# Optimization experiments

Hardware: AMD Instinct MI355X
Metric: run time of the kernel (lower is better)

The kernel has to match this reference:

```python
import math
import jax, jax.numpy as jnp
import numpy as np

NC, NA, NL = 80, 3, 3
NO = NC + 5
STRIDES = (8, 16, 32)
BS, IN_CH, IMG, NT = 8, 256, 640, 200
BALANCE = (4.0, 1.0, 0.25)
G, ANCHOR_T, EPS = 0.5, 2.91, 1e-9
LBOX_W, LOBJ_W, LCLS_W, POS_BAL = 0.05, 1.0, 0.5, 0.5
OFF = np.array([[0., 0.], [1., 0.], [0., 1.], [-1., 0.], [0., -1.]], np.float32) * G
_h = np.sqrt(np.array([0.5, 1.0, 2.0], np.float32))  # h_ratios = sqrt(aspect_ratios)
# per layer anchors: (w, h) = (size/h_ratio, size*h_ratio), divided by stride (grid units)
ANCHORS = np.stack([np.stack([s / _h, s * _h], 1) / st
                    for s, st in zip((32., 64., 128.), STRIDES)]).astype(np.float32)  # [NL,NA,2]


def setup_inputs():
    key = jax.random.key(0)
    ks = jax.random.split(key, 16)
    inp = {}
    for i, st in enumerate(STRIDES):
        n = IMG // st
        inp[f"feat{i}"] = jax.random.normal(ks[i], (BS, IN_CH, n, n), jnp.float32)
        inp[f"w{i}"] = jax.random.normal(ks[3 + i], (NO * NA, IN_CH), jnp.float32) * 0.02
        b = np.zeros((NA, NO), np.float32)
        b[:, 4] += math.log(8 / (640 / st) ** 2)          # _initialize_biases obj prior
        b[:, 5:] += math.log(0.6 / (NC - 0.99))           # _initialize_biases cls prior
        inp[f"b{i}"] = jnp.asarray(b.reshape(-1))
    # targets: [NT, 6] = (image_idx, class, cx, cy, w, h) normalized to [0,1]
    img = jax.random.randint(ks[6], (NT, 1), 0, BS).astype(jnp.float32)
    cls = jax.random.randint(ks[7], (NT, 1), 0, NC).astype(jnp.float32)
    xy = jax.random.uniform(ks[8], (NT, 2), minval=0.05, maxval=0.95)
    wh = jax.random.uniform(ks[9], (NT, 2), minval=0.02, maxval=0.3)
    inp["targets"] = jnp.concatenate([img, cls, xy, wh], 1)
    return inp


def _head(x, w, b):
    # 1x1 conv == channel GEMM, then view/permute to [bs, na, ny, nx, no]
    y = jnp.einsum('bchw,oc->bohw', x, w) + b[None, :, None, None]
    bs, _, ny, nx = y.shape
    return y.reshape(bs, NA, NO, ny, nx).transpose(0, 1, 3, 4, 2)


def _ciou(b1, b2):
    # b1, b2: [n,4] in center-xywh format; YOLOv5-style CIoU
    x1, y1, w1, h1 = b1[:, 0], b1[:, 1], b1[:, 2], b1[:, 3]
    x2, y2, w2, h2 = b2[:, 0], b2[:, 1], b2[:, 2], b2[:, 3]
    b1x1, b1x2, b1y1, b1y2 = x1 - w1 / 2, x1 + w1 / 2, y1 - h1 / 2, y1 + h1 / 2
    b2x1, b2x2, b2y1, b2y2 = x2 - w2 / 2, x2 + w2 / 2, y2 - h2 / 2, y2 + h2 / 2
    inter = (jnp.maximum(jnp.minimum(b1x2, b2x2) - jnp.maximum(b1x1, b2x1), 0.0)
             * jnp.maximum(jnp.minimum(b1y2, b2y2) - jnp.maximum(b1y1, b2y1), 0.0))
    union = w1 * h1 + w2 * h2 - inter + EPS
    iou = inter / union
    cw = jnp.maximum(b1x2, b2x2) - jnp.minimum(b1x1, b2x1)  # enclosing box
    ch = jnp.maximum(b1y2, b2y2) - jnp.minimum(b1y1, b2y1)
    c2 = cw ** 2 + ch ** 2 + EPS
    rho2 = ((b2x1 + b2x2 - b1x1 - b1x2) ** 2 + (b2y1 + b2y2 - b1y1 - b1y2) ** 2) / 4
    v = (4.0 / math.pi ** 2) * (jnp.arctan(w2 / (h2 + EPS)) - jnp.arctan(w1 / (h1 + EPS))) ** 2
    alpha = jax.lax.stop_gradient(v / (v - iou + (1.0 + EPS)))
    return iou - (rho2 / c2 + v * alpha)


def _bce_pw(logits, t, pw):
    # BCEWithLogits with pos_weight: pw*t*(-logsigmoid(x)) + (1-t)*softplus(x)
    return pw * t * jax.nn.softplus(-logits) + (1.0 - t) * jax.nn.softplus(logits)


def _forward(feats, ws, bias, targets):
    anchors = jnp.asarray(ANCHORS)
    off = jnp.asarray(OFF)
    ai = jnp.arange(NA, dtype=jnp.float32)
    # targets replicated per anchor with anchor index appended: [NA, NT, 7]
    tg = jnp.concatenate([jnp.broadcast_to(targets[None], (NA, NT, 6)),
                          jnp.broadcast_to(ai[:, None, None], (NA, NT, 1))], 2)
    lbox = jnp.float32(0.0); lobj = jnp.float32(0.0); lcls = jnp.float32(0.0)
    for i in range(NL):
        pi = _head(feats[i], ws[i], bias[i])  # [BS, NA, ny, nx, NO]
        ny, nx = pi.shape[2], pi.shape[3]
        gain = jnp.array([1, 1, nx, ny, nx, ny, 1], jnp.float32)
        t = tg * gain  # grid units, [NA, NT, 7]
        # anchor-ratio filter (torch: t = t[j]) expressed as a validity mask
        r = t[..., 4:6] / anchors[i][:, None, :]
        m_anchor = (jnp.max(jnp.maximum(r, 1.0 / r), -1) < ANCHOR_T).reshape(-1)  # [NA*NT]
        tf = t.reshape(-1, 7)
        gxy = tf[:, 2:4]
        gxi = jnp.array([nx, ny], jnp.float32) - gxy
        near = (gxy % 1.0 < G) & (gxy > 1.0)
        far = (gxi % 1.0 < G) & (gxi > 1.0)
        sel = jnp.stack([jnp.ones_like(near[:, 0]), near[:, 0], near[:, 1], far[:, 0], far[:, 1]])
        mask = (sel & m_anchor[None]).reshape(-1)  # [5*NA*NT] valid candidates
        N = tf.shape[0]
        t5 = jnp.broadcast_to(tf[None], (5, N, 7)).reshape(-1, 7)
        offs = jnp.broadcast_to(off[:, None, :], (5, N, 2)).reshape(-1, 2)
        b_idx = t5[:, 0].astype(jnp.int32)
        c_idx = t5[:, 1].astype(jnp.int32)
        a_idx = t5[:, 6].astype(jnp.int32)
        gxy5, gwh5 = t5[:, 2:4], t5[:, 4:6]
        gij = (gxy5 - offs).astype(jnp.int32)  # trunc, values are positive -> matches .long()
        gi = jnp.clip(gij[:, 0], 0, nx - 1)
        gj = jnp.clip(gij[:, 1], 0, ny - 1)
        tbox = jnp.concatenate([gxy5 - gij.astype(jnp.float32), gwh5], 1)
        anch = anchors[i][a_idx]
        # gather predictions at sparse (b, a, gj, gi)
        ps = pi[b_idx, a_idx, gj, gi]  # [M, NO]
        pxy = jax.nn.sigmoid(ps[:, :2]) * 2.0 - 0.5
        pwh = (jax.nn.sigmoid(ps[:, 2:4]) * 2.0) ** 2 * anch
        iou = _ciou(jnp.concatenate([pxy, pwh], 1), tbox)
        fmask = mask.astype(jnp.float32)
        n_valid = fmask.sum()
        lbox = lbox + jnp.sum(fmask * (1.0 - iou)) / jnp.maximum(n_valid, 1.0)
        # scatter tobj; invalid rows routed to padded batch slot BS then sliced off
        b_s = jnp.where(mask, b_idx, BS)
        tobj = jnp.zeros((BS + 1, NA, ny, nx), jnp.float32)
        tobj = tobj.at[b_s, a_idx, gj, gi].set(
            jax.lax.stop_gradient(jnp.maximum(iou, 0.0)))[:BS]
        # classification BCE with dynamically computed pos_weight
        tcl = jax.nn.one_hot(c_idx, NC, dtype=jnp.float32)
        pw_c = (n_valid * (NC - 1)) * POS_BAL / jnp.maximum(n_valid, 2.0)
        bce_c = _bce_pw(ps[:, 5:], tcl, pw_c)
        lcls = lcls + jnp.sum(fmask[:, None] * bce_c) / jnp.maximum(n_valid * NC, 1.0)
        # objectness BCE over the full map with dynamic pos_weight
        fg_o = (tobj > 0).sum().astype(jnp.float32)
        bg_o = (tobj == 0).sum().astype(jnp.float32)
        pw_o = bg_o * POS_BAL / jnp.maximum(fg_o, 2.0)
        lobj = lobj + jnp.mean(_bce_pw(pi[..., 4], tobj, pw_o)) * BALANCE[i]
    return jnp.stack([lbox * LBOX_W, lobj * LOBJ_W, lcls * LCLS_W])


def reference(feat0, feat1, feat2, w0, w1, w2, b0, b1, b2, targets):
    return _forward((feat0, feat1, feat2), (w0, w1, w2), (b0, b1, b2), targets)
```

## Files before the change

kernel.cpp:

```cpp
#include <hip/hip_runtime.h>
#include <stdint.h>

#define NCLS 80
#define NO 85
#define CIN 256
#define ANCHOR_T 2.91f
#define EPSF 1e-9f

#define S0 153600
#define S1_ 38400
#define S2_ 9600
#define LB0 0
#define LB1 153600
#define LB2 192000

#define NGATHB 375
#define NHEADB 1050
#define NB (NGATHB + NHEADB)
#define NREC (NGATHB * 24)
#define NFIN1 96

#define WS_TOBJ_OFF 0
#define WS_HSP_OFF  806400
#define WS_GP_OFF   810608
#define WS_REC_OFF  816608
#define WS_PART_OFF 960608

__device__ __constant__ float AW_[3] = {5.656854249f, 4.0f, 2.828427125f};
__device__ __constant__ float AH_[3] = {2.828427125f, 4.0f, 5.656854249f};

__device__ __forceinline__ float softplusf(float x) {
    return fmaxf(x, 0.0f) + log1pf(expf(-fabsf(x)));
}
__device__ __forceinline__ float sigmoidf_(float x) {
    return 1.0f / (1.0f + expf(-x));
}
__device__ __forceinline__ float wave_red(float v) {
    #pragma unroll
    for (int o = 32; o > 0; o >>= 1) v += __shfl_down(v, o);
    return v;
}

struct HeadSm {
    float lw[3][CIN];
    float part[16][16][13];
    float ws_[4];
};
struct GathSm {
    float lf[8][260];
    float pb[8][3][5];
    float tbx[8][4];
    int   vm[8], eb[8], egi[8], egj[8], ec[8];
    int   kblk;
    float r1[24], r2[24];
    float wsum[2][4];
};
union AllSm { HeadSm h; GathSm g; };

template<int PERQ, int BLK0>
__device__ __forceinline__ void head_impl(
    const float* __restrict__ f, const float* __restrict__ w, const float* __restrict__ bi,
    float* __restrict__ hsp, int hb, int tid, HeadSm& sm)
{
    for (int i = tid; i < 3 * CIN; i += 256) {
        int a = i >> 8, c = i & 255;
        sm.lw[a][c] = w[(a * NO + 4) * CIN + c];
    }
    __syncthreads();

    const int q     = tid & 15;
    const int chunk = tid >> 4;
    const int qL = (hb - BLK0) * 16 + q;
    const int b  = qL / PERQ;
    const int r  = qL - b * PERQ;
    const float4* p = (const float4*)f + (b * CIN + chunk * 16) * PERQ + r;

    float acc[12];
    #pragma unroll
    for (int j = 0; j < 12; ++j) acc[j] = 0.f;

    #pragma unroll
    for (int i = 0; i < 16; ++i) {
        float4 v = p[i * PERQ];
        const int c = chunk * 16 + i;
        #pragma unroll
        for (int a = 0; a < 3; ++a) {
            float wv = sm.lw[a][c];
            acc[a*4+0] += v.x * wv;
            acc[a*4+1] += v.y * wv;
            acc[a*4+2] += v.z * wv;
            acc[a*4+3] += v.w * wv;
        }
    }

    #pragma unroll
    for (int v = 0; v < 12; ++v) sm.part[chunk][q][v] = acc[v];
    __syncthreads();

    float sp = 0.f;
    if (tid < 192) {
        int q2 = tid / 12, v = tid - q2 * 12;
        float s = 0.f;
        #pragma unroll
        for (int c2 = 0; c2 < 16; ++c2) s += sm.part[c2][q2][v];
        s += bi[(v >> 2) * NO + 4];
        sp = softplusf(s);
    }
    sp = wave_red(sp);
    if ((tid & 63) == 0) sm.ws_[tid >> 6] = sp;
    __syncthreads();
    if (tid == 0)
        hsp[hb] = sm.ws_[0] + sm.ws_[1] + sm.ws_[2] + sm.ws_[3];
}

__device__ void gath_impl(
    const float* __restrict__ f, const float* __restrict__ w, const float* __restrict__ bi,
    const float* __restrict__ targets,
    unsigned* __restrict__ tobj4, float4* __restrict__ gp, int4* __restrict__ recs,
    int bid, int tid, int l, int o, int tile, GathSm& sm)
{
    const int nx = (l == 0) ? 80 : (l == 1) ? 40 : 20;
    const int ny = nx;
    const int plane = nx * ny;
    const int ltb = (l == 0) ? LB0 : (l == 1) ? LB1 : LB2;

    if (tid < 8) {
        const int t = tid;
        const int n = tile * 8 + t;
        const float* tg = targets + n * 6;
        float tb = tg[0], tcl = tg[1];
        float gx = tg[2] * (float)nx, gy = tg[3] * (float)ny;
        float gw = tg[4] * (float)nx, gh = tg[5] * (float)ny;
        float ox = 0.f, oy = 0.f;
        bool s = true;
        if (o == 1)      { s = (fmodf(gx, 1.f) < 0.5f) && (gx > 1.f); ox = 0.5f; }
        else if (o == 2) { s = (fmodf(gy, 1.f) < 0.5f) && (gy > 1.f); oy = 0.5f; }
        else if (o == 3) { float gxi = (float)nx - gx; s = (fmodf(gxi, 1.f) < 0.5f) && (gxi > 1.f); ox = -0.5f; }
        else if (o == 4) { float gyi = (float)ny - gy; s = (fmodf(gyi, 1.f) < 0.5f) && (gyi > 1.f); oy = -0.5f; }
        int vmask = 0;
        if (s) {
            #pragma unroll
            for (int a = 0; a < 3; ++a) {
                float rw = gw / AW_[a], rh = gh / AH_[a];
                float mr = fmaxf(fmaxf(rw, 1.f / rw), fmaxf(rh, 1.f / rh));
                if (mr < ANCHOR_T) vmask |= (1 << a);
            }
        }
        sm.vm[t] = vmask;
        int gi = (int)(gx - ox);
        int gj = (int)(gy - oy);
        sm.tbx[t][0] = gx - (float)gi;
        sm.tbx[t][1] = gy - (float)gj;
        sm.tbx[t][2] = gw;
        sm.tbx[t][3] = gh;
        sm.egi[t] = min(max(gi, 0), nx - 1);
        sm.egj[t] = min(max(gj, 0), ny - 1);
        sm.eb[t]  = (int)tb;
        sm.ec[t]  = (int)tcl;
    }
    __syncthreads();

    if (tid == 0) {
        int k = 0;
        #pragma unroll
        for (int t = 0; t < 8; ++t) k |= sm.vm[t];
        sm.kblk = k;
    }
    __syncthreads();

    if (sm.kblk == 0) {
        if (tid == 0) gp[bid] = make_float4(0.f, 0.f, 0.f, 0.f);
        return;
    }

    {
        const int t  = tid >> 5;
        const int ln = tid & 31;
        if (sm.vm[t]) {
            const float* fb = f + sm.eb[t] * CIN * plane + sm.egj[t] * nx + sm.egi[t];
            #pragma unroll
            for (int k2 = 0; k2 < 8; ++k2) {
                int c = ln + k2 * 32;
                sm.lf[t][c] = fb[c * plane];
            }
        }
    }
    __syncthreads();

    float s1 = 0.f, s2 = 0.f;
    if (tid < 255) {
        const int a  = tid / 85;
        const int oc = tid - a * 85;
        const float bv = bi[tid];
        float dacc[8];
        #pragma unroll
        for (int t = 0; t < 8; ++t) dacc[t] = bv;
        const float4* wr4 = (const float4*)w + tid * 64;
        #pragma unroll 4
        for (int c4 = 0; c4 < 64; ++c4) {
            float4 wv = wr4[c4];
            #pragma unroll
            for (int t = 0; t < 8; ++t) {
                float4 fv = *((const float4*)&sm.lf[t][c4 * 4]);
                dacc[t] += wv.x * fv.x + wv.y * fv.y + wv.z * fv.z + wv.w * fv.w;
            }
        }
        if (oc >= 5) {
            const int cls = oc - 5;
            #pragma unroll
            for (int t = 0; t < 8; ++t) {
                if ((sm.vm[t] >> a) & 1) {
                    if (cls == sm.ec[t]) s1 += softplusf(-dacc[t]);
                    else                 s2 += softplusf(dacc[t]);
                }
            }
        } else {
            #pragma unroll
            for (int t = 0; t < 8; ++t) sm.pb[t][a][oc] = dacc[t];
        }
    }
    s1 = wave_red(s1);
    s2 = wave_red(s2);
    if ((tid & 63) == 0) { sm.wsum[0][tid >> 6] = s1; sm.wsum[1][tid >> 6] = s2; }
    __syncthreads();

    if (tid < 24) {
        const int t = tid & 7;
        const int a = tid >> 3;
        if ((sm.vm[t] >> a) & 1) {
            float px = sigmoidf_(sm.pb[t][a][0]) * 2.f - 0.5f;
            float py = sigmoidf_(sm.pb[t][a][1]) * 2.f - 0.5f;
            float swp = sigmoidf_(sm.pb[t][a][2]) * 2.f; float pw = swp * swp * AW_[a];
            float shp = sigmoidf_(sm.pb[t][a][3]) * 2.f; float ph = shp * shp * AH_[a];
            float tx = sm.tbx[t][0], ty = sm.tbx[t][1], tw = sm.tbx[t][2], th = sm.tbx[t][3];
            float b1x1 = px - pw * 0.5f, b1x2 = px + pw * 0.5f;
            float b1y1 = py - ph * 0.5f, b1y2 = py + ph * 0.5f;
            float b2x1 = tx - tw * 0.5f, b2x2 = tx + tw * 0.5f;
            float b2y1 = ty - th * 0.5f, b2y2 = ty + th * 0.5f;
            float iw = fmaxf(fminf(b1x2, b2x2) - fmaxf(b1x1, b2x1), 0.f);
            float ih = fmaxf(fminf(b1y2, b2y2) - fmaxf(b1y1, b2y1), 0.f);
            float inter = iw * ih;
            float uni = pw * ph + tw * th - inter + EPSF;
            float iou = inter / uni;
            float cw = fmaxf(b1x2, b2x2) - fminf(b1x1, b2x1);
            float chh = fmaxf(b1y2, b2y2) - fminf(b1y1, b2y1);
            float c2 = cw * cw + chh * chh + EPSF;
            float dx = b2x1 + b2x2 - b1x1 - b1x2;
            float dy = b2y1 + b2y2 - b1y1 - b1y2;
            float rho2 = (dx * dx + dy * dy) * 0.25f;
            float dat = atanf(tw / (th + EPSF)) - atanf(pw / (ph + EPSF));
            float v = 0.4052847346f * dat * dat;
            float alpha = v / (v - iou + (1.f + EPSF));
            float ciou = iou - (rho2 / c2 + v * alpha);
            float tt = fmaxf(ciou, 0.f);
            int idx = ltb + ((sm.eb[t] * 3 + a) * ny + sm.egj[t]) * nx + sm.egi[t];
            int n = tile * 8 + t;
            int ek = o * 600 + a * 200 + n;
            int slot = bid * 24 + tid;
            int4 rc; rc.x = idx; rc.y = __float_as_int(sm.pb[t][a][4]); rc.z = __float_as_int(tt); rc.w = 1;
            recs[slot] = rc;
            unsigned pk = 0xC0000000u | ((unsigned)(ek + 1) << 14) | (unsigned)slot;
            atomicMax(&tobj4[idx], pk);
            sm.r1[tid] = 1.f - ciou;
            sm.r2[tid] = 1.f;
        } else {
            sm.r1[tid] = 0.f;
            sm.r2[tid] = 0.f;
        }
    }
    __syncthreads();
    if (tid == 0) {
        float lb = 0.f, nv = 0.f;
        #pragma unroll
        for (int e = 0; e < 24; ++e) { lb += sm.r1[e]; nv += sm.r2[e]; }
        float4 gpv;
        gpv.x = lb; gpv.y = nv;
        gpv.z = sm.wsum[0][0] + sm.wsum[0][1] + sm.wsum[0][2] + sm.wsum[0][3];
        gpv.w = sm.wsum[1][0] + sm.wsum[1][1] + sm.wsum[1][2] + sm.wsum[1][3];
        gp[bid] = gpv;
    }
}

__global__ __launch_bounds__(256) void yolo_main(
    const float* __restrict__ f0, const float* __restrict__ w0, const float* __restrict__ b0,
    const float* __restrict__ f1, const float* __restrict__ w1, const float* __restrict__ b1,
    const float* __restrict__ f2, const float* __restrict__ w2, const float* __restrict__ b2,
    const float* __restrict__ targets,
    unsigned* __restrict__ tobj4, float* __restrict__ hsp,
    float4* __restrict__ gp, int4* __restrict__ recs)
{
    __shared__ AllSm sm;
    const int bid = blockIdx.x;
    const int tid = threadIdx.x;

    if (bid < NGATHB) {
        const int l    = bid / 125;
        const int rem  = bid - l * 125;
        const int o    = rem / 25;
        const int tile = rem - o * 25;
        const float* f  = (l == 0) ? f0 : (l == 1) ? f1 : f2;
        const float* w  = (l == 0) ? w0 : (l == 1) ? w1 : w2;
        const float* bi = (l == 0) ? b0 : (l == 1) ? b1 : b2;
        gath_impl(f, w, bi, targets, tobj4, gp, recs, bid, tid, l, o, tile, sm.g);
    } else {
        const int hb = bid - NGATHB;
        if (hb < 800)       head_impl<1600, 0>  (f0, w0, b0, hsp, hb, tid, sm.h);
        else if (hb < 1000) head_impl<400, 800> (f1, w1, b1, hsp, hb, tid, sm.h);
        else                head_impl<100, 1000>(f2, w2, b2, hsp, hb, tid, sm.h);
    }
}

__global__ __launch_bounds__(256) void yolo_fin1(
    unsigned* __restrict__ tobj4, const float* __restrict__ hsp,
    const float4* __restrict__ gp, const int4* __restrict__ recs,
    float* __restrict__ part)
{
    const int bid = blockIdx.x, tid = threadIdx.x;
    __shared__ float red[24];
    if (tid < 24) red[tid] = 0.f;
    __syncthreads();

    float t2b[3] = {0,0,0};
    for (int i = bid * 256 + tid; i < NHEADB; i += NFIN1 * 256) {
        int l = (i < 800) ? 0 : (i < 1000) ? 1 : 2;
        t2b[l] += hsp[i];
    }
    float lb[3] = {0,0,0}, nv[3] = {0,0,0}, c1[3] = {0,0,0}, c2[3] = {0,0,0};
    for (int i = bid * 256 + tid; i < NGATHB; i += NFIN1 * 256) {
        int l = i / 125;
        float4 g = gp[i];
        lb[l] += g.x; nv[l] += g.y; c1[l] += g.z; c2[l] += g.w;
    }
    float T1[3] = {0,0,0}, T2s[3] = {0,0,0}, fgc[3] = {0,0,0};
    for (int i = bid * 256 + tid; i < NREC; i += NFIN1 * 256) {
        int4 r = recs[i];
        if (r.w != 1) continue;
        unsigned old = atomicExch(&tobj4[r.x], 0u);
        if (old >= 0xC0000000u) {
            int wsl = (int)(old & 0x3FFFu);
            float tw = __int_as_float(recs[wsl].z);
            float x  = __int_as_float(r.y);
            int l = (r.x >= LB2) ? 2 : (r.x >= LB1) ? 1 : 0;
            T1[l]  += tw * softplusf(-x);
            T2s[l] += tw * softplusf(x);
            fgc[l] += (tw > 0.f) ? 1.f : 0.f;
        }
    }
    #pragma unroll
    for (int l = 0; l < 3; ++l) {
        if (lb[l]  != 0.f) atomicAdd(&red[l*8+0], lb[l]);
        if (nv[l]  != 0.f) atomicAdd(&red[l*8+1], nv[l]);
        if (c1[l]  != 0.f) atomicAdd(&red[l*8+2], c1[l]);
        if (c2[l]  != 0.f) atomicAdd(&red[l*8+3], c2[l]);
        if (t2b[l] != 0.f) atomicAdd(&red[l*8+4], t2b[l]);
        if (T1[l]  != 0.f) atomicAdd(&red[l*8+5], T1[l]);
        if (T2s[l] != 0.f) atomicAdd(&red[l*8+6], T2s[l]);
        if (fgc[l] != 0.f) atomicAdd(&red[l*8+7], fgc[l]);
    }
    __syncthreads();
    if (tid < 24) part[bid * 24 + tid] = red[tid];
}

__global__ __launch_bounds__(256) void yolo_fin2(
    const float* __restrict__ part, float* __restrict__ out)
{
    const int tid = threadIdx.x;
    __shared__ float red[24];
    if (tid < 24) red[tid] = 0.f;
    __syncthreads();
    if (tid < 240) {
        int j = tid % 24;
        float s = 0.f;
        for (int b = tid / 24; b < NFIN1; b += 10) s += part[b * 24 + j];
        atomicAdd(&red[j], s);
    }
    __syncthreads();
    if (tid == 0) {
        const float bal[3]   = {4.f, 1.f, 0.25f};
        const float numel[3] = {(float)S0, (float)S1_, (float)S2_};
        float lbox = 0.f, lobj = 0.f, lcls = 0.f;
        for (int i = 0; i < 3; ++i) {
            float lbs = red[i*8+0];
            float nvv = red[i*8+1];
            float s1  = red[i*8+2];
            float s2  = red[i*8+3];
            float T2b = red[i*8+4];
            float T1v = red[i*8+5];
            float T2  = T2b - red[i*8+6];
            float fg  = red[i*8+7];
            lbox += lbs / fmaxf(nvv, 1.f);
            float pwc = nvv * (float)(NCLS - 1) * 0.5f / fmaxf(nvv, 2.f);
            lcls += (pwc * s1 + s2) / fmaxf(nvv * (float)NCLS, 1.f);
            float bg = numel[i] - fg;
            float pwo = bg * 0.5f / fmaxf(fg, 2.f);
            lobj += (pwo * T1v + T2) / numel[i] * bal[i];
        }
        out[0] = lbox * 0.05f;
        out[1] = lobj * 1.0f;
        out[2] = lcls * 0.5f;
    }
}

extern "C" void kernel_launch(void* const* d_in, const int* in_sizes, int n_in,
                              void* d_out, int out_size, void* d_ws, size_t ws_size,
                              hipStream_t stream) {
    (void)in_sizes; (void)n_in; (void)out_size; (void)ws_size;
    const float* f0 = (const float*)d_in[0];
    const float* w0 = (const float*)d_in[1];
    const float* b0 = (const float*)d_in[2];
    const float* f1 = (const float*)d_in[3];
    const float* w1 = (const float*)d_in[4];
    const float* b1 = (const float*)d_in[5];
    const float* f2 = (const float*)d_in[6];
    const float* w2 = (const float*)d_in[7];
    const float* b2 = (const float*)d_in[8];
    const float* tg = (const float*)d_in[9];
    float* out = (float*)d_out;

    char* ws = (char*)d_ws;
    unsigned* tobj4 = (unsigned*)(ws + WS_TOBJ_OFF);
    float* hsp      = (float*)(ws + WS_HSP_OFF);
    float4* gp      = (float4*)(ws + WS_GP_OFF);
    int4* recs      = (int4*)(ws + WS_REC_OFF);
    float* part     = (float*)(ws + WS_PART_OFF);

    yolo_main<<<dim3(NB), dim3(256), 0, stream>>>(f0, w0, b0, f1, w1, b1, f2, w2, b2, tg,
                                                  tobj4, hsp, gp, recs);
    yolo_fin1<<<dim3(NFIN1), dim3(256), 0, stream>>>(tobj4, hsp, gp, recs, part);
    yolo_fin2<<<dim3(1), dim3(256), 0, stream>>>(part, out);
}
```

Before: 162.0 us.

## Split objectness head into 4x more blocks with shuffle-based channel reduction

The objectness-head blocks now each handle 4 quads instead of 16, with 64 channel groups of 4 channels per thread. Partial sums are reduced with wave shuffles and a small shared array, which removes the large shared partial buffer and one barrier. This gives four times as many blocks, which raises parallelism and memory-level concurrency but also adds more per-block weight loads and more hsp entries for the finalizer. Bounds checks were also added to the tobj record processing.

Measured after the change: 159.5 us. No clear change (-1.5%).

```diff
diff --git a/kernel.cpp b/kernel.cpp
--- a/kernel.cpp
+++ b/kernel.cpp
@@ -13,18 +13,19 @@
 #define LB0 0
 #define LB1 153600
 #define LB2 192000
+#define TOTCELL 201600
 
 #define NGATHB 375
-#define NHEADB 1050
+#define NHEADB 4200
 #define NB (NGATHB + NHEADB)
 #define NREC (NGATHB * 24)
 #define NFIN1 96
 
 #define WS_TOBJ_OFF 0
 #define WS_HSP_OFF  806400
-#define WS_GP_OFF   810608
-#define WS_REC_OFF  816608
-#define WS_PART_OFF 960608
+#define WS_GP_OFF   823200
+#define WS_REC_OFF  829200
+#define WS_PART_OFF 973200
 
 __device__ __constant__ float AW_[3] = {5.656854249f, 4.0f, 2.828427125f};
 __device__ __constant__ float AH_[3] = {2.828427125f, 4.0f, 5.656854249f};
@@ -41,12 +42,11 @@
     return v;
 }
 
-struct HeadSm {
+struct __align__(16) HeadSm {
     float lw[3][CIN];
-    float part[16][16][13];
-    float ws_[4];
+    float wpart[4][4][12];
 };
-struct GathSm {
+struct __align__(16) GathSm {
     float lf[8][260];
     float pb[8][3][5];
     float tbx[8][4];
@@ -55,7 +55,7 @@
     float r1[24], r2[24];
     float wsum[2][4];
 };
-union AllSm { HeadSm h; GathSm g; };
+union __align__(16) AllSm { HeadSm h; GathSm g; };
 
 template<int PERQ, int BLK0>
 __device__ __forceinline__ void head_impl(
@@ -68,49 +68,59 @@
     }
     __syncthreads();
 
-    const int q     = tid & 15;
-    const int chunk = tid >> 4;
-    const int qL = (hb - BLK0) * 16 + q;
-    const int b  = qL / PERQ;
-    const int r  = qL - b * PERQ;
-    const float4* p = (const float4*)f + (b * CIN + chunk * 16) * PERQ + r;
+    const int q   = tid & 3;
+    const int c16 = tid >> 2;
+    const int qL  = (hb - BLK0) * 4 + q;
+    const int b   = qL / PERQ;
+    const int r   = qL - b * PERQ;
+    const float4* p = (const float4*)f + (b * CIN + c16 * 4) * PERQ + r;
+
+    float4 v0 = p[0];
+    float4 v1 = p[PERQ];
+    float4 v2 = p[2 * PERQ];
+    float4 v3 = p[3 * PERQ];
 
     float acc[12];
+    const int c0 = c16 * 4;
     #pragma unroll
-    for (int j = 0; j < 12; ++j) acc[j] = 0.f;
+    for (int a = 0; a < 3; ++a) {
+        float w0_ = sm.lw[a][c0 + 0];
+        float w1_ = sm.lw[a][c0 + 1];
+        float w2_ = sm.lw[a][c0 + 2];
+        float w3_ = sm.lw[a][c0 + 3];
+        acc[a*4+0] = v0.x * w0_ + v1.x * w1_ + v2.x * w2_ + v3.x * w3_;
+        acc[a*4+1] = v0.y * w0_ + v1.y * w1_ + v2.y * w2_ + v3.y * w3_;
+        acc[a*4+2] = v0.z * w0_ + v1.z * w1_ + v2.z * w2_ + v3.z * w3_;
+        acc[a*4+3] = v0.w * w0_ + v1.w * w1_ + v2.w * w2_ + v3.w * w3_;
+    }
 
     #pragma unroll
-    for (int i = 0; i < 16; ++i) {
-        float4 v = p[i * PERQ];
-        const int c = chunk * 16 + i;
+    for (int j = 0; j < 12; ++j) {
+        float v = acc[j];
+        v += __shfl_xor(v, 4);
+        v += __shfl_xor(v, 8);
+        v += __shfl_xor(v, 16);
+        v += __shfl_xor(v, 32);
+        acc[j] = v;
+    }
+    const int wv = tid >> 6;
+    const int ln = tid & 63;
+    if (ln < 4) {
         #pragma unroll
-        for (int a = 0; a < 3; ++a) {
-            float wv = sm.lw[a][c];
-            acc[a*4+0] += v.x * wv;
-            acc[a*4+1] += v.y * wv;
-            acc[a*4+2] += v.z * wv;
-            acc[a*4+3] += v.w * wv;
-        }
-    }
-
-    #pragma unroll
-    for (int v = 0; v < 12; ++v) sm.part[chunk][q][v] = acc[v];
+        for (int j = 0; j < 12; ++j) sm.wpart[wv][ln][j] = acc[j];
+    }
     __syncthreads();
 
     float sp = 0.f;
-    if (tid < 192) {
+    if (tid < 48) {
         int q2 = tid / 12, v = tid - q2 * 12;
-        float s = 0.f;
-        #pragma unroll
-        for (int c2 = 0; c2 < 16; ++c2) s += sm.part[c2][q2][v];
-        s += bi[(v >> 2) * NO + 4];
+        float s = sm.wpart[0][q2][v] + sm.wpart[1][q2][v]
+                + sm.wpart[2][q2][v] + sm.wpart[3][q2][v]
+                + bi[(v >> 2) * NO + 4];
         sp = softplusf(s);
     }
     sp = wave_red(sp);
-    if ((tid & 63) == 0) sm.ws_[tid >> 6] = sp;
-    __syncthreads();
-    if (tid == 0)
-        hsp[hb] = sm.ws_[0] + sm.ws_[1] + sm.ws_[2] + sm.ws_[3];
+    if (tid == 0) hsp[hb] = sp;
 }
 
 __device__ void gath_impl(
@@ -304,9 +314,9 @@
         gath_impl(f, w, bi, targets, tobj4, gp, recs, bid, tid, l, o, tile, sm.g);
     } else {
         const int hb = bid - NGATHB;
-        if (hb < 800)       head_impl<1600, 0>  (f0, w0, b0, hsp, hb, tid, sm.h);
-        else if (hb < 1000) head_impl<400, 800> (f1, w1, b1, hsp, hb, tid, sm.h);
-        else                head_impl<100, 1000>(f2, w2, b2, hsp, hb, tid, sm.h);
+        if (hb < 3200)      head_impl<1600, 0>   (f0, w0, b0, hsp, hb, tid, sm.h);
+        else if (hb < 4000) head_impl<400, 3200> (f1, w1, b1, hsp, hb, tid, sm.h);
+        else                head_impl<100, 4000> (f2, w2, b2, hsp, hb, tid, sm.h);
     }
 }
 
@@ -322,7 +332,7 @@
 
     float t2b[3] = {0,0,0};
     for (int i = bid * 256 + tid; i < NHEADB; i += NFIN1 * 256) {
-        int l = (i < 800) ? 0 : (i < 1000) ? 1 : 2;
+        int l = (i < 3200) ? 0 : (i < 4000) ? 1 : 2;
         t2b[l] += hsp[i];
     }
     float lb[3] = {0,0,0}, nv[3] = {0,0,0}, c1[3] = {0,0,0}, c2[3] = {0,0,0};
@@ -335,15 +345,18 @@
     for (int i = bid * 256 + tid; i < NREC; i += NFIN1 * 256) {
         int4 r = recs[i];
         if (r.w != 1) continue;
+        if (r.x < 0 || r.x >= TOTCELL) continue;
         unsigned old = atomicExch(&tobj4[r.x], 0u);
         if (old >= 0xC0000000u) {
             int wsl = (int)(old & 0x3FFFu);
-            float tw = __int_as_float(recs[wsl].z);
-            float x  = __int_as_float(r.y);
-            int l = (r.x >= LB2) ? 2 : (r.x >= LB1) ? 1 : 0;
-            T1[l]  += tw * softplusf(-x);
-            T2s[l] += tw * softplusf(x);
-            fgc[l] += (tw > 0.f) ? 1.f : 0.f;
+            if (wsl < NREC) {
+                float tw = __int_as_float(recs[wsl].z);
+                float x  = __int_as_float(r.y);
+                int l = (r.x >= LB2) ? 2 : (r.x >= LB1) ? 1 : 0;
+                T1[l]  += tw * softplusf(-x);
+                T2s[l] += tw * softplusf(x);
+                fgc[l] += (tw > 0.f) ? 1.f : 0.f;
+            }
         }
     }
     #pragma unroll
```
